# Kernel optimization log

Hardware: AMD Instinct MI355X
Metric: run time of the kernel (lower is better)

## Reference

```python
import jax, jax.numpy as jnp
import numpy as np
from jax import lax

EPS = 1e-5

def setup_inputs() -> dict:
    key = jax.random.key(0)
    ks = jax.random.split(key, 8)
    B, D, H, W = 2, 96, 96, 96
    K, N, R = 4, 16, 6
    return {
        "x": jax.random.normal(ks[0], (B, D, H, W), jnp.float32),
        "x_proj_weight": jax.random.normal(ks[1], (K, R + 2 * N, D), jnp.float32) * 0.05,
        "dt_projs_weight": jax.random.normal(ks[2], (K, D, R), jnp.float32) * 0.05,
        "dt_projs_bias": jax.random.normal(ks[3], (K, D), jnp.float32) * 0.05,
        "A_logs": jax.random.uniform(ks[4], (K * D, N), jnp.float32, 0.0, 1.0),
        "Ds": jax.random.normal(ks[5], (K * D,), jnp.float32) * 0.1,
        "norm_weight": jnp.ones((D,), jnp.float32),
        "norm_bias": jnp.zeros((D,), jnp.float32),
    }

def _cross_scan(x):
    # x: [B,C,H,W] -> xs: [B,4,C,L]; dirs: row-major, col-major, and their flips
    B, C, H, W = x.shape
    x_hw = x.reshape(B, C, H * W)
    x_wh = jnp.swapaxes(x, 2, 3).reshape(B, C, H * W)
    return jnp.stack([x_hw, x_wh, x_hw[..., ::-1], x_wh[..., ::-1]], axis=1)

def _cross_merge(ys, H, W):
    # ys: [B,4,C,L] -> y: [B,C,L]
    B, K, C, L = ys.shape
    ys = ys[:, 0:2] + ys[:, 2:4][..., ::-1]
    y_wh = jnp.swapaxes(ys[:, 1].reshape(B, C, W, H), 2, 3).reshape(B, C, L)
    return ys[:, 0] + y_wh

def _forward(x, x_proj_weight, dt_projs_weight, dt_projs_bias, A_logs, Ds,
             norm_weight, norm_bias):
    B, D, H, W = x.shape
    L = H * W
    K, _, R = dt_projs_weight.shape
    N = A_logs.shape[1]

    xs = _cross_scan(x)                                        # [B,K,D,L]
    x_dbl = jnp.einsum('bkdl,kcd->bkcl', xs, x_proj_weight)    # [B,K,R+2N,L]
    dts, Bs, Cs = x_dbl[:, :, :R], x_dbl[:, :, R:R + N], x_dbl[:, :, R + N:]
    dts = jnp.einsum('bkrl,kdr->bkdl', dts, dt_projs_weight)   # [B,K,D,L]

    A = -jnp.exp(A_logs).reshape(K, D, N)                      # [K,D,N]
    delta = jax.nn.softplus(dts + dt_projs_bias[None, :, :, None])  # [B,K,D,L]

    # time-major for scan
    u_t = jnp.moveaxis(xs, 3, 0)       # [L,B,K,D]
    d_t = jnp.moveaxis(delta, 3, 0)    # [L,B,K,D]
    B_t = jnp.moveaxis(Bs, 3, 0)       # [L,B,K,N]
    C_t = jnp.moveaxis(Cs, 3, 0)       # [L,B,K,N]

    def step(h, inp):
        u, dlt, b, c = inp
        h = jnp.exp(dlt[..., None] * A) * h + (dlt * u)[..., None] * b[:, :, None, :]
        y = jnp.einsum('bkdn,bkn->bkd', h, c)
        return h, y

    h0 = jnp.zeros((B, K, D, N), xs.dtype)
    _, ys = lax.scan(step, h0, (u_t, d_t, B_t, C_t))           # ys: [L,B,K,D]
    ys = jnp.moveaxis(ys, 0, 3)                                # [B,K,D,L]
    ys = ys + Ds.reshape(1, K, D, 1) * xs                      # skip term

    y = _cross_merge(ys, H, W)                                 # [B,D,L]
    y = jnp.swapaxes(y, 1, 2)                                  # [B,L,D]
    # out_norm: LayerNorm over channel dim
    mu = y.mean(-1, keepdims=True)
    var = y.var(-1, keepdims=True)
    y = (y - mu) / jnp.sqrt(var + EPS) * norm_weight + norm_bias
    return y.reshape(B, H, W, D)

def reference(x, x_proj_weight, dt_projs_weight, dt_projs_bias, A_logs, Ds,
              norm_weight, norm_bias):
    return _forward(x, x_proj_weight, dt_projs_weight, dt_projs_bias,
                    A_logs, Ds, norm_weight, norm_bias)
```

## Files before the change

### kernel.cpp

```cpp
#include <hip/hip_runtime.h>
#include <hip/hip_bf16.h>
#include <hip/hip_fp16.h>


constexpr int Bn = 2, Kn = 4, Dn = 96, Hn = 96, Wn = 96, Ln = Hn * Wn;
constexpr int Nn = 16, Rn = 6;
constexpr int CCn = 288, CLn = 32;

#define DI __device__ __forceinline__

typedef _Float16 half2v __attribute__((ext_vector_type(2)));

DI float bf2f(unsigned short u) { return __uint_as_float(((unsigned)u) << 16); }
DI bool probe_bf16(const void* nw) { return ((const unsigned*)nw)[0] == 0x3F803F80u; }
DI float ld_in(const void* p, long i, bool bf) {
  return bf ? bf2f(((const unsigned short*)p)[i]) : ((const float*)p)[i];
}
DI float fexp2(float x) {
#if __has_builtin(__builtin_amdgcn_exp2f)
  return __builtin_amdgcn_exp2f(x);
#else
  return exp2f(x);
#endif
}
DI float softplus_fast(float v) {
  return (v > 15.f) ? v : __logf(1.f + __expf(v));
}
DI float dot2acc(unsigned a, unsigned b, float c) {
#if __has_builtin(__builtin_amdgcn_fdot2)
  half2v av, bv;
  __builtin_memcpy(&av, &a, 4);
  __builtin_memcpy(&bv, &b, 4);
  return __builtin_amdgcn_fdot2(av, bv, c, false);
#else
  __half2 ah = *(__half2*)&a, bh = *(__half2*)&b;
  float2 af = __half22float2(ah), bf2_ = __half22float2(bh);
  return fmaf(af.y, bf2_.y, fmaf(af.x, bf2_.x, c));
#endif
}
DI float quad_reduce_add(float v) {
  int a = __builtin_amdgcn_mov_dpp(__float_as_int(v), 0xB1, 0xF, 0xF, true);
  v += __int_as_float(a);
  int b = __builtin_amdgcn_mov_dpp(__float_as_int(v), 0x4E, 0xF, 0xF, true);
  v += __int_as_float(b);
  return v;
}
constexpr float LOG2E = 1.44269504088896340736f;
constexpr int DLS = 98;

__global__ __launch_bounds__(256) void k_prep(
    const void* __restrict__ x, const void* __restrict__ xpw,
    const void* __restrict__ dtw, const void* __restrict__ dtb,
    const void* __restrict__ Al, const void* __restrict__ Ds,
    const void* __restrict__ nw, const void* __restrict__ nb,
    float* __restrict__ xl, float* __restrict__ xlT,
    __half* __restrict__ wp_h, unsigned* __restrict__ wdt_p,
    float* __restrict__ bias_f, float* __restrict__ Al_f,
    float* __restrict__ dsum, float* __restrict__ nw_f, float* __restrict__ nb_f) {
  __shared__ float tile[96 * 49];
  bool bf = probe_bf16(nw);
  int h = blockIdx.x, wh = blockIdx.y, b = blockIdx.z;
  int w0 = wh * 48;
  int tid = threadIdx.x;
  int fi = ((blockIdx.z * gridDim.y + blockIdx.y) * gridDim.x + blockIdx.x) *
               256 + tid;
  int fgs = gridDim.x * gridDim.y * gridDim.z * 256;
  for (int i = fi; i < Kn * 4000; i += fgs) {
    int k = i / 4000, r = i - k * 4000;
    int c = r / 100, dd = r - c * 100;
    wp_h[i] = __float2half(
        (c < 38 && dd < 96) ? ld_in(xpw, (long)k * 38 * 96 + c * 96 + dd, bf)
                            : 0.f);
  }
  for (int i = fi; i < Kn * Dn; i += fgs) {
    __half2 h01 = __floats2half2_rn(ld_in(dtw, (long)i * 6 + 0, bf),
                                    ld_in(dtw, (long)i * 6 + 1, bf));
    __half2 h23 = __floats2half2_rn(ld_in(dtw, (long)i * 6 + 2, bf),
                                    ld_in(dtw, (long)i * 6 + 3, bf));
    __half2 h45 = __floats2half2_rn(ld_in(dtw, (long)i * 6 + 4, bf),
                                    ld_in(dtw, (long)i * 6 + 5, bf));
    wdt_p[i * 4 + 0] = *(unsigned*)&h01;
    wdt_p[i * 4 + 1] = *(unsigned*)&h23;
    wdt_p[i * 4 + 2] = *(unsigned*)&h45;
    wdt_p[i * 4 + 3] = 0u;
    bias_f[i] = ld_in(dtb, i, bf);
  }
  for (int i = fi; i < Kn * Dn * Nn; i += fgs)
    Al_f[i] = -__expf(ld_in(Al, i, bf)) * LOG2E;
  for (int i = fi; i < Dn; i += fgs) {
    dsum[i] = ld_in(Ds, i, bf) + ld_in(Ds, 96 + i, bf) +
              ld_in(Ds, 192 + i, bf) + ld_in(Ds, 288 + i, bf);
    nw_f[i] = ld_in(nw, i, bf);
    nb_f[i] = ld_in(nb, i, bf);
  }
  long srcbase = (long)b * Dn * Ln + (long)h * 96 + w0;
  for (int i = tid; i < 96 * 48; i += 256) {
    int d = i / 48, w = i - d * 48;
    tile[d * 49 + w] = ld_in(x, srcbase + (long)d * Ln + w, bf);
  }
  __syncthreads();
  float* xlb = xl + (size_t)b * Ln * 96;
  float* xTb = xlT + (size_t)b * Ln * 96;
  for (int i = tid; i < 48 * 96; i += 256) {
    int w = i / 96, d = i - w * 96;
    float v = tile[d * 49 + w];
    xlb[(size_t)(h * 96 + w0 + w) * 96 + d] = v;
    xTb[(size_t)((w0 + w) * 96 + h) * 96 + d] = v;
  }
}

__global__ __launch_bounds__(256) void k_proj(
    const float* __restrict__ xl, const float* __restrict__ xlT,
    const __half* __restrict__ wp_h, const unsigned* __restrict__ wdt_p,
    const float* __restrict__ bias_f, const float* __restrict__ Al_f,
    __half2* __restrict__ ddu, __half* __restrict__ BCh,
    float* __restrict__ PSg) {
  constexpr int TL = 32;
  __shared__ __half xt[TL * 102];
  __shared__ __half wp[40 * 100];
  __shared__ __half xd2[TL * 40];
  __shared__ unsigned wdt_u[96 * 4];
  __shared__ float bias[96];
  int tile = blockIdx.x, k = blockIdx.y, b = blockIdx.z;
  int l0 = tile * TL;
  int tid = threadIdx.x;
  bool rev = (k & 2) != 0;

  {
    const uint4* wsrc = (const uint4*)(wp_h + (size_t)k * 4000);
    for (int i = tid; i < 500; i += 256) ((uint4*)wp)[i] = wsrc[i];
    const uint4* dsrc = (const uint4*)(wdt_p + (size_t)k * 384);
    for (int i = tid; i < 96; i += 256) ((uint4*)wdt_u)[i] = dsrc[i];
    if (tid < 96) bias[tid] = bias_f[k * 96 + tid];
  }
  {
    const float* xsrc = ((k & 1) ? xlT : xl) + (size_t)b * Ln * 96;
    for (int i = tid; i < TL * 24; i += 256) {
      int r = i / 24, q = i - r * 24;
      int g = rev ? (Ln - 1 - l0 - r) : (l0 + r);
      float4 v = *(const float4*)(xsrc + (size_t)g * 96 + q * 4);
      *(__half2*)(&xt[r * 102 + q * 4]) = __floats2half2_rn(v.x, v.y);
      *(__half2*)(&xt[r * 102 + q * 4 + 2]) = __floats2half2_rn(v.z, v.w);
    }
  }
  __syncthreads();

  {
    int jg = tid & 31, cg = tid >> 5;
    int c0 = cg * 5;
    float acc[5] = {0.f, 0.f, 0.f, 0.f, 0.f};
    for (int dd = 0; dd < 96; dd += 4) {
      uint2 xa = *(const uint2*)&xt[jg * 102 + dd];
#pragma unroll
      for (int i = 0; i < 5; ++i) {
        uint2 wv = *(const uint2*)&wp[(c0 + i) * 100 + dd];
        acc[i] = dot2acc(xa.x, wv.x, acc[i]);
        acc[i] = dot2acc(xa.y, wv.y, acc[i]);
      }
    }
#pragma unroll
    for (int i = 0; i < 5; ++i) xd2[jg * 40 + c0 + i] = __float2half(acc[i]);
  }
  __syncthreads();

  size_t bk = (size_t)b * 4 + k;
  {
    __half2* o = (__half2*)(BCh + (bk * (size_t)Ln + l0) * 32);
    for (int i = tid; i < TL * 16; i += 256) {
      int j = i >> 4, cp = i & 15;
      int c = cp * 2;
      int ng = c >> 3, idx = c & 7;
      int ch = (idx < 4) ? (6 + ng * 4 + idx) : (22 + ng * 4 + (idx - 4));
      o[i] = *(const __half2*)&xd2[j * 40 + ch];
    }
  }
  __half* delta_l = wp;
  if (tid < 192) {
    int d = tid >> 1, th = tid & 1;
    unsigned wv0 = wdt_u[d * 4], wv1 = wdt_u[d * 4 + 1], wv2 = wdt_u[d * 4 + 2];
    float bd = bias[d];
    int ts = th * 16;
#pragma unroll 4
    for (int t = ts; t < ts + 16; ++t) {
      uint2 xr01 = *(const uint2*)&xd2[t * 40];
      unsigned xr2 = *(const unsigned*)&xd2[t * 40 + 4];
      float v = dot2acc(xr01.x, wv0,
                dot2acc(xr01.y, wv1,
                dot2acc(xr2, wv2, bd)));
      delta_l[t * DLS + d] = __float2half(softplus_fast(v));
    }
  }
  __syncthreads();

  if (tid < 192) {
    int d = tid >> 1, hg = tid & 1;
    float ac2[8];
    *(float4*)&ac2[0] = *(const float4*)&Al_f[(k * 96 + d) * 16 + hg * 8];
    *(float4*)&ac2[4] = *(const float4*)&Al_f[(k * 96 + d) * 16 + hg * 8 + 4];
    float spsum = 0.f;
    float S[8] = {0.f, 0.f, 0.f, 0.f, 0.f, 0.f, 0.f, 0.f};
    __half2* dcol = ddu + (bk * (size_t)Ln + l0) * 96 + d;
#pragma unroll 2
    for (int t = 0; t < TL; ++t) {
      __half sph = delta_l[t * DLS + d];
      float spc = __half2float(sph);
      float u = __half2float(xt[t * 102 + d]);
      __half fyh = __float2half(spc * u);
      float fy = __half2float(fyh);
      if (hg == 0) dcol[(size_t)t * 96] = __halves2half2(sph, fyh);
      spsum += spc;
#pragma unroll
      for (int w = 0; w < 4; ++w) {
        unsigned bw = *(const unsigned*)&xd2[t * 40 + 6 + 8 * hg + 2 * w];
        float2 Bv = __half22float2(*(__half2*)&bw);
        float a0 = fexp2(spc * ac2[w * 2]);
        S[w * 2] = fmaf(a0, S[w * 2], fy * Bv.x);
        float a1 = fexp2(spc * ac2[w * 2 + 1]);
        S[w * 2 + 1] = fmaf(a1, S[w * 2 + 1], fy * Bv.y);
      }
    }
    float P[8];
#pragma unroll
    for (int j = 0; j < 8; ++j) P[j] = fexp2(spsum * ac2[j]);
    size_t ob = ((size_t)(bk * 96 + d) * CCn + tile) * 32 + hg * 8;
    *(float4*)&PSg[ob] = make_float4(P[0], P[1], P[2], P[3]);
    *(float4*)&PSg[ob + 4] = make_float4(P[4], P[5], P[6], P[7]);
    *(float4*)&PSg[ob + 16] = make_float4(S[0], S[1], S[2], S[3]);
    *(float4*)&PSg[ob + 20] = make_float4(S[4], S[5], S[6], S[7]);
  }
}

__global__ __launch_bounds__(256) void k_midscan(float* __restrict__ PSg) {
  __shared__ float Pl[256], Sl[256];
  int bkd = blockIdx.x;
  int tid = threadIdx.x;
  int g = tid >> 4, n = tid & 15;
  constexpr int CPG = CCn / 16;
  size_t base = ((size_t)bkd * CCn + (size_t)g * CPG) * 32 + n;
  float Pr[CPG], Sr[CPG];
#pragma unroll
  for (int i = 0; i < CPG; ++i) {
    Pr[i] = PSg[base + (size_t)i * 32];
    Sr[i] = PSg[base + (size_t)i * 32 + 16];
  }
  float Pa = 1.f, Sa = 0.f;
#pragma unroll
  for (int i = 0; i < CPG; ++i) { Sa = fmaf(Pr[i], Sa, Sr[i]); Pa *= Pr[i]; }
  Pl[tid] = Pa;
  Sl[tid] = Sa;
  __syncthreads();
#pragma unroll
  for (int s = 1; s < 16; s <<= 1) {
    float Pp = 1.f, Sp = 0.f;
    if (g >= s) { Pp = Pl[(g - s) * 16 + n]; Sp = Sl[(g - s) * 16 + n]; }
    __syncthreads();
    if (g >= s) {
      Sl[tid] = fmaf(Pl[tid], Sp, Sl[tid]);
      Pl[tid] *= Pp;
    }
    __syncthreads();
  }
  float h = (g == 0) ? 0.f : Sl[(g - 1) * 16 + n];
#pragma unroll
  for (int i = 0; i < CPG; ++i) {
    PSg[base + (size_t)i * 32] = h;
    h = fmaf(Pr[i], h, Sr[i]);
  }
}

__global__ __launch_bounds__(192) void k_scan2(
    const __half2* __restrict__ ddu, const __half* __restrict__ BCh,
    const float* __restrict__ Al_f, const float* __restrict__ PSg,
    __half* __restrict__ ysH) {
  __shared__ __half2 dd_s[CLn * 96];
  __shared__ __half bc_s[CLn * 32];
  int chunk = blockIdx.x, k = blockIdx.y, b = blockIdx.z;
  int tid = threadIdx.x;
  int dp = tid >> 2, ng = tid & 3;
  int d0 = dp * 2, n0 = ng * 4;
  int bk = b * 4 + k;
  int t0 = chunk * CLn;
  float ac[2][4];
#pragma unroll
  for (int dd = 0; dd < 2; ++dd)
#pragma unroll
    for (int j = 0; j < 4; ++j)
      ac[dd][j] = Al_f[(k * 96 + d0 + dd) * 16 + n0 + j];
  {
    const uint4* dsrc = (const uint4*)(ddu + ((size_t)bk * Ln + t0) * 96);
    uint4* ddst = (uint4*)dd_s;
    for (int i = tid; i < CLn * 96 / 4; i += 192) ddst[i] = dsrc[i];
    const uint4* bsrc = (const uint4*)(BCh + ((size_t)bk * Ln + t0) * 32);
    uint4* bdst = (uint4*)bc_s;
    for (int i = tid; i < CLn * 32 * 2 / 16; i += 192) bdst[i] = bsrc[i];
  }
  float4 ha = *(const float4*)(PSg + ((size_t)(bk * 96 + d0) * CCn + chunk) * 32 + n0);
  float4 hb = *(const float4*)(PSg + ((size_t)(bk * 96 + d0 + 1) * CCn + chunk) * 32 + n0);
  float h[2][4] = {{ha.x, ha.y, ha.z, ha.w}, {hb.x, hb.y, hb.z, hb.w}};
  __syncthreads();

#pragma unroll 2
  for (int t = 0; t < CLn; ++t) {
    union { uint2 u; __half2 h2[2]; } dv;
    dv.u = *(const uint2*)&dd_s[t * 96 + d0];
    union { uint4 u; __half2 h2[4]; } bc;
    bc.u = *(const uint4*)&bc_s[t * 32 + ng * 8];
    float2 f0 = __half22float2(dv.h2[0]);
    float2 f1 = __half22float2(dv.h2[1]);
    float2 b01 = __half22float2(bc.h2[0]);
    float2 b23 = __half22float2(bc.h2[1]);
    float2 c01 = __half22float2(bc.h2[2]);
    float2 c23 = __half22float2(bc.h2[3]);
    float Ba[4] = {b01.x, b01.y, b23.x, b23.y};
    float Ca[4] = {c01.x, c01.y, c23.x, c23.y};
    float py0 = 0.f, py1 = 0.f;
#pragma unroll
    for (int j = 0; j < 4; ++j) {
      float a0 = fexp2(f0.x * ac[0][j]);
      h[0][j] = fmaf(a0, h[0][j], f0.y * Ba[j]);
      py0 = fmaf(h[0][j], Ca[j], py0);
      float a1 = fexp2(f1.x * ac[1][j]);
      h[1][j] = fmaf(a1, h[1][j], f1.y * Ba[j]);
      py1 = fmaf(h[1][j], Ca[j], py1);
    }
    py0 = quad_reduce_add(py0);
    py1 = quad_reduce_add(py1);
    if (ng == 0)
      *(__half2*)&ysH[((size_t)bk * Ln + t0 + t) * 96 + d0] =
          __halves2half2(__float2half(py0), __float2half(py1));
  }
}

__global__ __launch_bounds__(256) void k_merge_ln(
    const __half* __restrict__ ysH, const float* __restrict__ xl,
    const float* __restrict__ dsum, const void* __restrict__ nwraw,
    const float* __restrict__ nw_f, const float* __restrict__ nb_f,
    void* __restrict__ outv) {
  __shared__ float yt[32 * 98];
  __shared__ float nwf[96], nbf[96], dsm[96], mu_s[32], rs_s[32];
  bool bf = probe_bf16(nwraw);
  int tile = blockIdx.x, b = blockIdx.y;
  int h0 = (tile / 12) * 4, w0 = (tile % 12) * 8;
  int tid = threadIdx.x;
  if (tid < 96) {
    nwf[tid] = nw_f[tid];
    nbf[tid] = nb_f[tid];
    dsm[tid] = dsum[tid];
  }
  const __half* y0 = ysH + (size_t)(b * 4 + 0) * Ln * 96;
  const __half* y1 = ysH + (size_t)(b * 4 + 1) * Ln * 96;
  const __half* y2 = ysH + (size_t)(b * 4 + 2) * Ln * 96;
  const __half* y3 = ysH + (size_t)(b * 4 + 3) * Ln * 96;
  const float* xb = xl + (size_t)b * Ln * 96;
  __syncthreads();
  for (int i = tid; i < 32 * 48; i += 256) {
    int rr = i / 48, dp = i - rr * 48, d = dp * 2;
    int hh = h0 + (rr >> 3), ww = w0 + (rr & 7);
    int l = hh * 96 + ww, t1 = ww * 96 + hh;
    float2 v0 = __half22float2(*(const __half2*)&y0[(size_t)l * 96 + d]);
    float2 v1 = __half22float2(*(const __half2*)&y1[(size_t)t1 * 96 + d]);
    float2 v2 = __half22float2(*(const __half2*)&y2[(size_t)(Ln - 1 - l) * 96 + d]);
    float2 v3 = __half22float2(*(const __half2*)&y3[(size_t)(Ln - 1 - t1) * 96 + d]);
    float2 xv = *(const float2*)&xb[(size_t)l * 96 + d];
    float2 r;
    r.x = v0.x + v1.x + v2.x + v3.x + dsm[d] * xv.x;
    r.y = v0.y + v1.y + v2.y + v3.y + dsm[d + 1] * xv.y;
    *(float2*)&yt[rr * 98 + d] = r;
  }
  __syncthreads();
  {
    int rr = tid >> 3, qq = tid & 7;
    float s = 0.f, ss = 0.f;
#pragma unroll 4
    for (int j = 0; j < 12; ++j) {
      float v = yt[rr * 98 + qq * 12 + j];
      s += v;
      ss += v * v;
    }
#pragma unroll
    for (int m = 1; m < 8; m <<= 1) {
      s += __shfl_xor(s, m, 64);
      ss += __shfl_xor(ss, m, 64);
    }
    if (qq == 0) {
      float mu = s * (1.f / 96.f);
      float var = fmaxf(ss * (1.f / 96.f) - mu * mu, 0.f);
      mu_s[rr] = mu;
      rs_s[rr] = rsqrtf(var + 1e-5f);
    }
  }
  __syncthreads();
  for (int i = tid; i < 32 * 48; i += 256) {
    int rr = i / 48, dp = i - rr * 48, d = dp * 2;
    int hh = h0 + (rr >> 3), ww = w0 + (rr & 7);
    size_t idx = ((size_t)b * Ln + hh * 96 + ww) * 96 + d;
    float2 yv = *(const float2*)&yt[rr * 98 + d];
    float mu = mu_s[rr], rs = rs_s[rr];
    float o0 = (yv.x - mu) * rs * nwf[d] + nbf[d];
    float o1 = (yv.y - mu) * rs * nwf[d + 1] + nbf[d + 1];
    if (bf) {
      union { unsigned u; unsigned short us[2]; } pk;
      __hip_bfloat16 b0 = __float2bfloat16(o0), b1 = __float2bfloat16(o1);
      pk.us[0] = *(unsigned short*)&b0;
      pk.us[1] = *(unsigned short*)&b1;
      *(unsigned*)&((__hip_bfloat16*)outv)[idx] = pk.u;
    } else {
      *(float2*)&((float*)outv)[idx] = make_float2(o0, o1);
    }
  }
}

extern "C" void kernel_launch(void* const* d_in, const int* in_sizes, int n_in,
                              void* d_out, int out_size, void* d_ws, size_t ws_size,
                              hipStream_t stream) {
  const void* x   = d_in[0];
  const void* xpw = d_in[1];
  const void* dtw = d_in[2];
  const void* dtb = d_in[3];
  const void* Al  = d_in[4];
  const void* Ds  = d_in[5];
  const void* nw  = d_in[6];
  const void* nb  = d_in[7];

  char* ws = (char*)d_ws;
  size_t off = 0;
  auto alloc = [&](size_t bytes) {
    char* p = ws + off;
    off += (bytes + 511) & ~(size_t)511;
    return p;
  };
  float* xl    = (float*)alloc((size_t)Bn * Ln * Dn * 4);
  float* xlT   = (float*)alloc((size_t)Bn * Ln * Dn * 4);
  __half* wp_h = (__half*)alloc((size_t)Kn * 4000 * 2);
  unsigned* wdt_p = (unsigned*)alloc((size_t)Kn * Dn * 4 * 4);
  float* bias_f= (float*)alloc((size_t)Kn * Dn * 4);
  float* Al_f  = (float*)alloc((size_t)Kn * Dn * Nn * 4);
  float* dsum  = (float*)alloc((size_t)Dn * 4);
  float* nw_f  = (float*)alloc((size_t)Dn * 4);
  float* nb_f  = (float*)alloc((size_t)Dn * 4);
  __half2* ddu = (__half2*)alloc((size_t)Bn * Kn * Ln * Dn * 4);
  __half* BCh  = (__half*)alloc((size_t)Bn * Kn * Ln * 32 * 2);
  float* PS    = (float*)alloc((size_t)Bn * Kn * Dn * CCn * 32 * 4);
  __half* ysH  = (__half*)alloc((size_t)Bn * Kn * Ln * Dn * 2);
  (void)ws_size; (void)in_sizes; (void)n_in; (void)out_size;

  k_prep<<<dim3(Hn, 2, Bn), dim3(256), 0, stream>>>(
      x, xpw, dtw, dtb, Al, Ds, nw, nb, xl, xlT, wp_h, wdt_p, bias_f, Al_f,
      dsum, nw_f, nb_f);
  k_proj<<<dim3(Ln / 32, Kn, Bn), dim3(256), 0, stream>>>(
      xl, xlT, wp_h, wdt_p, bias_f, Al_f, ddu, BCh, PS);
  k_midscan<<<dim3(Bn * Kn * Dn), dim3(256), 0, stream>>>(PS);
  k_scan2<<<dim3(CCn, Kn, Bn), dim3(192), 0, stream>>>(ddu, BCh, Al_f, PS, ysH);
  k_merge_ln<<<dim3(288, Bn), dim3(256), 0, stream>>>(ysH, xl, dsum, nw, nw_f,
                                                      nb_f, d_out);
}
```

Baseline: 171.5 us.

## Store transposed input copies in fp16 and transpose delta LDS layout

The two channel-last input copies (xl, xlT) written by k_prep are now stored as fp16 instead of fp32. This halves their global write and read traffic in k_prep, k_proj and k_merge_ln, and removes a conversion in k_proj. The per-tile delta buffer in shared memory is also switched from time-major to channel-major with stride 33, which changes its bank-access pattern. The cost is that the skip term in the merge kernel now reads x rounded to fp16, adding a small precision loss.

```diff
diff --git a/kernel.cpp b/kernel.cpp
--- a/kernel.cpp
+++ b/kernel.cpp
@@ -46,14 +46,14 @@
   return v;
 }
 constexpr float LOG2E = 1.44269504088896340736f;
-constexpr int DLS = 98;
+constexpr int DLT = 33;
 
 __global__ __launch_bounds__(256) void k_prep(
     const void* __restrict__ x, const void* __restrict__ xpw,
     const void* __restrict__ dtw, const void* __restrict__ dtb,
     const void* __restrict__ Al, const void* __restrict__ Ds,
     const void* __restrict__ nw, const void* __restrict__ nb,
-    float* __restrict__ xl, float* __restrict__ xlT,
+    __half* __restrict__ xl, __half* __restrict__ xlT,
     __half* __restrict__ wp_h, unsigned* __restrict__ wdt_p,
     float* __restrict__ bias_f, float* __restrict__ Al_f,
     float* __restrict__ dsum, float* __restrict__ nw_f, float* __restrict__ nb_f) {
@@ -99,18 +99,19 @@
     tile[d * 49 + w] = ld_in(x, srcbase + (long)d * Ln + w, bf);
   }
   __syncthreads();
-  float* xlb = xl + (size_t)b * Ln * 96;
-  float* xTb = xlT + (size_t)b * Ln * 96;
-  for (int i = tid; i < 48 * 96; i += 256) {
-    int w = i / 96, d = i - w * 96;
-    float v = tile[d * 49 + w];
-    xlb[(size_t)(h * 96 + w0 + w) * 96 + d] = v;
-    xTb[(size_t)((w0 + w) * 96 + h) * 96 + d] = v;
+  __half* xlb = xl + (size_t)b * Ln * 96;
+  __half* xTb = xlT + (size_t)b * Ln * 96;
+  for (int i = tid; i < 48 * 48; i += 256) {
+    int w = i / 48, dp = i - w * 48;
+    int d = dp * 2;
+    __half2 v = __floats2half2_rn(tile[d * 49 + w], tile[(d + 1) * 49 + w]);
+    *(__half2*)&xlb[(size_t)(h * 96 + w0 + w) * 96 + d] = v;
+    *(__half2*)&xTb[(size_t)((w0 + w) * 96 + h) * 96 + d] = v;
   }
 }
 
 __global__ __launch_bounds__(256) void k_proj(
-    const float* __restrict__ xl, const float* __restrict__ xlT,
+    const __half* __restrict__ xl, const __half* __restrict__ xlT,
     const __half* __restrict__ wp_h, const unsigned* __restrict__ wdt_p,
     const float* __restrict__ bias_f, const float* __restrict__ Al_f,
     __half2* __restrict__ ddu, __half* __restrict__ BCh,
@@ -134,13 +135,14 @@
     if (tid < 96) bias[tid] = bias_f[k * 96 + tid];
   }
   {
-    const float* xsrc = ((k & 1) ? xlT : xl) + (size_t)b * Ln * 96;
+    const __half* xsrc = ((k & 1) ? xlT : xl) + (size_t)b * Ln * 96;
     for (int i = tid; i < TL * 24; i += 256) {
       int r = i / 24, q = i - r * 24;
       int g = rev ? (Ln - 1 - l0 - r) : (l0 + r);
-      float4 v = *(const float4*)(xsrc + (size_t)g * 96 + q * 4);
-      *(__half2*)(&xt[r * 102 + q * 4]) = __floats2half2_rn(v.x, v.y);
-      *(__half2*)(&xt[r * 102 + q * 4 + 2]) = __floats2half2_rn(v.z, v.w);
+      uint2 v = *(const uint2*)(xsrc + (size_t)g * 96 + q * 4);
+      unsigned* dst = (unsigned*)&xt[r * 102 + q * 4];
+      dst[0] = v.x;
+      dst[1] = v.y;
     }
   }
   __syncthreads();
@@ -187,7 +189,7 @@
       float v = dot2acc(xr01.x, wv0,
                 dot2acc(xr01.y, wv1,
                 dot2acc(xr2, wv2, bd)));
-      delta_l[t * DLS + d] = __float2half(softplus_fast(v));
+      delta_l[d * DLT + t] = __float2half(softplus_fast(v));
     }
   }
   __syncthreads();
@@ -202,7 +204,7 @@
     __half2* dcol = ddu + (bk * (size_t)Ln + l0) * 96 + d;
 #pragma unroll 2
     for (int t = 0; t < TL; ++t) {
-      __half sph = delta_l[t * DLS + d];
+      __half sph = delta_l[d * DLT + t];
       float spc = __half2float(sph);
       float u = __half2float(xt[t * 102 + d]);
       __half fyh = __float2half(spc * u);
@@ -332,7 +334,7 @@
 }
 
 __global__ __launch_bounds__(256) void k_merge_ln(
-    const __half* __restrict__ ysH, const float* __restrict__ xl,
+    const __half* __restrict__ ysH, const __half* __restrict__ xl,
     const float* __restrict__ dsum, const void* __restrict__ nwraw,
     const float* __restrict__ nw_f, const float* __restrict__ nb_f,
     void* __restrict__ outv) {
@@ -351,7 +353,7 @@
   const __half* y1 = ysH + (size_t)(b * 4 + 1) * Ln * 96;
   const __half* y2 = ysH + (size_t)(b * 4 + 2) * Ln * 96;
   const __half* y3 = ysH + (size_t)(b * 4 + 3) * Ln * 96;
-  const float* xb = xl + (size_t)b * Ln * 96;
+  const __half* xb = xl + (size_t)b * Ln * 96;
   __syncthreads();
   for (int i = tid; i < 32 * 48; i += 256) {
     int rr = i / 48, dp = i - rr * 48, d = dp * 2;
@@ -361,7 +363,7 @@
     float2 v1 = __half22float2(*(const __half2*)&y1[(size_t)t1 * 96 + d]);
     float2 v2 = __half22float2(*(const __half2*)&y2[(size_t)(Ln - 1 - l) * 96 + d]);
     float2 v3 = __half22float2(*(const __half2*)&y3[(size_t)(Ln - 1 - t1) * 96 + d]);
-    float2 xv = *(const float2*)&xb[(size_t)l * 96 + d];
+    float2 xv = __half22float2(*(const __half2*)&xb[(size_t)l * 96 + d]);
     float2 r;
     r.x = v0.x + v1.x + v2.x + v3.x + dsm[d] * xv.x;
     r.y = v0.y + v1.y + v2.y + v3.y + dsm[d + 1] * xv.y;
@@ -429,8 +431,8 @@
     off += (bytes + 511) & ~(size_t)511;
     return p;
   };
-  float* xl    = (float*)alloc((size_t)Bn * Ln * Dn * 4);
-  float* xlT   = (float*)alloc((size_t)Bn * Ln * Dn * 4);
+  __half* xl   = (__half*)alloc((size_t)Bn * Ln * Dn * 2);
+  __half* xlT  = (__half*)alloc((size_t)Bn * Ln * Dn * 2);
   __half* wp_h = (__half*)alloc((size_t)Kn * 4000 * 2);
   unsigned* wdt_p = (unsigned*)alloc((size_t)Kn * Dn * 4 * 4);
   float* bias_f= (float*)alloc((size_t)Kn * Dn * 4);
```

After: 170.3 us. About the same (-0.7%).
